# Kernel tuning notes

Measured on AMD Instinct MI355X. Metric: run time of the kernel, lower is better.

The kernel has to match this reference:

```python
import jax, jax.numpy as jnp
import numpy as np

DIM = 768
HEADS = 12
HEAD_DIM = DIM // HEADS
SCALE = HEAD_DIM ** -0.5


def setup_inputs() -> dict:
    key = jax.random.key(0)
    k1, k2, k3, k4 = jax.random.split(key, 4)
    x = jax.random.normal(k1, (1, 4096, DIM), dtype=jnp.float32)
    # qkv: Linear(dim, 3*dim), bias=False
    W_qkv = jax.random.normal(k2, (DIM, 3 * DIM), dtype=jnp.float32) * (DIM ** -0.5)
    # proj: Linear(dim, dim) with bias
    W_proj = jax.random.normal(k3, (DIM, DIM), dtype=jnp.float32) * (DIM ** -0.5)
    b_proj = jax.random.normal(k4, (DIM,), dtype=jnp.float32) * 0.01
    return {"x": x, "W_qkv": W_qkv, "W_proj": W_proj, "b_proj": b_proj}


def reference(x, W_qkv, W_proj, b_proj):
    b, n, d = x.shape
    qkv = x @ W_qkv                                  # [b, n, 3d]
    q, k, v = jnp.split(qkv, 3, axis=-1)             # each [b, n, d]
    # split heads: [b, n, (h hd)] -> [b, h, n, hd]
    def heads(t):
        return t.reshape(b, n, HEADS, HEAD_DIM).transpose(0, 2, 1, 3)
    q, k, v = heads(q) * SCALE, heads(k), heads(v)
    sim = jnp.einsum('bhid,bhjd->bhij', q, k)        # [b, h, n, n] -- full score matrix
    attn = jax.nn.softmax(sim, axis=-1)
    out = jnp.einsum('bhij,bhjd->bhid', attn, v)     # [b, h, n, hd]
    out = out.transpose(0, 2, 1, 3).reshape(b, n, d)  # merge heads
    return out @ W_proj + b_proj
```

## Files before the change

### kernel.cpp

```cpp
#include <hip/hip_runtime.h>
#include <math.h>

#define TOKENS 4096
#define DMODEL 768
#define NHEADS 12
#define HDIM   64
#define QKV_N  2304
#define ATTN_SCALE 0.125f
#define QSCALE_LOG2E (0.125f * 1.44269504088896340736f)

typedef __attribute__((ext_vector_type(8))) short bf16x8;
typedef __attribute__((ext_vector_type(4))) float floatx4;

__device__ __forceinline__ ushort f2bf(float f) {
    union { float f; unsigned u; } cv; cv.f = f;
    unsigned u = cv.u;
    u += 0x7fffu + ((u >> 16) & 1u);
    return (ushort)(u >> 16);
}

__device__ __forceinline__ unsigned cvt_pk_bf16(float a, float b) {
    unsigned r;
    asm("v_cvt_pk_bf16_f32 %0, %1, %2" : "=v"(r) : "v"(a), "v"(b));
    return r;
}

__device__ __forceinline__ void gl2lds16(const ushort* g, ushort* l) {
    __builtin_amdgcn_global_load_lds(
        (const __attribute__((address_space(1))) void*)g,
        (__attribute__((address_space(3))) void*)l, 16, 0, 0);
}

__device__ __forceinline__ bf16x8 frag(const ushort* ls, int row, int chunk) {
    return *(const bf16x8*)(ls + row * 64 + ((chunk ^ (row & 7)) * 8));
}

__global__ __launch_bounds__(256) void cvt_bf16_kernel(
    const float* __restrict__ in, ushort* __restrict__ out, int n4)
{
    const int i = blockIdx.x * 256 + threadIdx.x;
    if (i < n4) {
        const float4 v = ((const float4*)in)[i];
        ushort4 h;
        h.x = f2bf(v.x); h.y = f2bf(v.y); h.z = f2bf(v.z); h.w = f2bf(v.w);
        ((ushort4*)out)[i] = h;
    }
}

__global__ __launch_bounds__(256) void transpose_cvt_kernel(
    const float* __restrict__ in, ushort* __restrict__ out, int R, int C)
{
    __shared__ ushort tile[32][33];
    const int tx  = threadIdx.x & 31;
    const int ty8 = threadIdx.x >> 5;
    const int c0 = blockIdx.x * 32;
    const int r0 = blockIdx.y * 32;
    #pragma unroll
    for (int p = 0; p < 4; ++p) {
        const int r = ty8 + p * 8;
        tile[r][tx] = f2bf(in[(size_t)(r0 + r) * C + c0 + tx]);
    }
    __syncthreads();
    #pragma unroll
    for (int p = 0; p < 4; ++p) {
        const int c = ty8 + p * 8;
        out[(size_t)(c0 + c) * R + r0 + tx] = tile[tx][c];
    }
}

template<int NT>
__device__ __forceinline__ void gemm_body_async(
    const ushort* __restrict__ A, const ushort* __restrict__ Bt, int K,
    int m0, int n0, floatx4 acc[4][NT], ushort* ls)
{
    ushort* lsA = ls;
    ushort* lsB = ls + 8192;

    const int tid  = threadIdx.x;
    const int lane = tid & 63;
    const int wave = tid >> 6;
    const int wm = wave >> 1, wn = wave & 1;
    const int quad = lane >> 4, l16 = lane & 15;

    const int lrow = lane >> 3;
    const int csw  = ((lane & 7) ^ lrow) * 8;

    const ushort* gA = A  + (size_t)(m0 + wave * 32 + lrow) * K + csw;
    const ushort* gB = Bt + (size_t)(n0 + wave * NT * 8 + lrow) * K + csw;
    ushort* lA = lsA + (wave * 32) * 64;
    ushort* lB = lsB + (wave * NT * 8) * 64;

    for (int k0 = 0; k0 < K; k0 += 64) {
        __syncthreads();
        #pragma unroll
        for (int p = 0; p < 4; ++p)
            gl2lds16(gA + (size_t)p * 8 * K + k0, lA + p * 8 * 64);
        #pragma unroll
        for (int p = 0; p < NT; ++p)
            gl2lds16(gB + (size_t)p * 8 * K + k0, lB + p * 8 * 64);
        __syncthreads();

        #pragma unroll
        for (int ks = 0; ks < 2; ++ks) {
            bf16x8 af[4], bfr[NT];
            #pragma unroll
            for (int mt = 0; mt < 4; ++mt)
                af[mt] = frag(lsA, wm * 64 + mt * 16 + l16, ks * 4 + quad);
            #pragma unroll
            for (int nt = 0; nt < NT; ++nt)
                bfr[nt] = frag(lsB, wn * NT * 16 + nt * 16 + l16, ks * 4 + quad);
            #pragma unroll
            for (int mt = 0; mt < 4; ++mt)
                #pragma unroll
                for (int nt = 0; nt < NT; ++nt)
                    acc[mt][nt] = __builtin_amdgcn_mfma_f32_16x16x32_bf16(
                        af[mt], bfr[nt], acc[mt][nt], 0, 0, 0);
        }
    }
}

__global__ __launch_bounds__(256) void gemm_qkv_mfma(
    const ushort* __restrict__ Xb, const ushort* __restrict__ Wt,
    ushort* __restrict__ Qb, ushort* __restrict__ Kb, ushort* __restrict__ Vt)
{
    __shared__ __align__(16) ushort ls[16384];
    const int m0 = blockIdx.y * 128;
    const int n0 = blockIdx.x * 128;

    floatx4 acc[4][4] = {};
    gemm_body_async<4>(Xb, Wt, DMODEL, m0, n0, acc, ls);

    const int tid  = threadIdx.x;
    const int lane = tid & 63;
    const int wave = tid >> 6;
    const int wm = wave >> 1, wn = wave & 1;
    const int quad = lane >> 4, l16 = lane & 15;

    if (n0 < 2 * DMODEL) {
        const float scale = (n0 < DMODEL) ? QSCALE_LOG2E : 1.0f;
        ushort* outp = (n0 < DMODEL) ? Qb : Kb;
        const int colg = (n0 < DMODEL) ? n0 : n0 - DMODEL;
        #pragma unroll
        for (int p = 0; p < 2; ++p) {
            __syncthreads();
            if (wm == p) {
                #pragma unroll
                for (int mt = 0; mt < 4; ++mt)
                    #pragma unroll
                    for (int nt = 0; nt < 4; ++nt) {
                        const int row = mt * 16 + quad * 4;
                        const int col = wn * 64 + nt * 16 + l16;
                        #pragma unroll
                        for (int r = 0; r < 4; ++r)
                            ls[(row + r) * 136 + col] = f2bf(acc[mt][nt][r] * scale);
                    }
            }
            __syncthreads();
            #pragma unroll
            for (int p2 = 0; p2 < 4; ++p2) {
                const int row = (tid >> 4) + p2 * 16;
                const int c8  = (tid & 15) * 8;
                *(uint4*)(outp + (size_t)(m0 + p * 64 + row) * DMODEL + colg + c8) =
                    *(const uint4*)(ls + row * 136 + c8);
            }
        }
    } else {
        const int hd0 = n0 - 2 * DMODEL;
        #pragma unroll
        for (int p = 0; p < 2; ++p) {
            __syncthreads();
            if (wn == p) {
                #pragma unroll
                for (int mt = 0; mt < 4; ++mt)
                    #pragma unroll
                    for (int nt = 0; nt < 4; ++nt) {
                        const int hd  = nt * 16 + l16;
                        const int tok = wm * 64 + mt * 16 + quad * 4;
                        #pragma unroll
                        for (int r = 0; r < 4; ++r)
                            ls[hd * 136 + tok + r] = f2bf(acc[mt][nt][r]);
                    }
            }
            __syncthreads();
            #pragma unroll
            for (int p2 = 0; p2 < 4; ++p2) {
                const int row = (tid >> 4) + p2 * 16;
                const int c8  = (tid & 15) * 8;
                *(uint4*)(Vt + (size_t)(hd0 + p * 64 + row) * TOKENS + m0 + c8) =
                    *(const uint4*)(ls + row * 136 + c8);
            }
        }
    }
}

__global__ __launch_bounds__(256) void gemm_proj_mfma(
    const ushort* __restrict__ Ab, const ushort* __restrict__ Wt,
    const float* __restrict__ bias, float* __restrict__ out)
{
    __shared__ __align__(16) ushort ls[12288];
    const int m0 = blockIdx.y * 128;
    const int n0 = blockIdx.x * 64;

    floatx4 acc[4][2] = {};
    gemm_body_async<2>(Ab, Wt, DMODEL, m0, n0, acc, ls);

    const int lane = threadIdx.x & 63;
    const int wave = threadIdx.x >> 6;
    const int wm = wave >> 1, wn = wave & 1;
    const int quad = lane >> 4, l16 = lane & 15;
    const int row0 = m0 + wm * 64 + quad * 4;
    const int col0 = n0 + wn * 32;

    #pragma unroll
    for (int nt = 0; nt < 2; ++nt) {
        const int col = col0 + nt * 16 + l16;
        const float bv = bias[col];
        #pragma unroll
        for (int mt = 0; mt < 4; ++mt)
            #pragma unroll
            for (int r = 0; r < 4; ++r)
                out[(size_t)(row0 + mt * 16 + r) * DMODEL + col] =
                    acc[mt][nt][r] + bv;
    }
}

__global__ __launch_bounds__(256) void attn_mfma_kernel(
    const ushort* __restrict__ Qb, const ushort* __restrict__ Kb,
    const ushort* __restrict__ Vt, ushort* __restrict__ attn_out)
{
    __shared__ __align__(16) ushort lds[16384];

    const int tid  = threadIdx.x;
    const int wave = tid >> 6;
    const int lane = tid & 63;
    const int quad = lane >> 4;
    const int l16  = lane & 15;
    const int h    = blockIdx.y;
    const int i0   = blockIdx.x * 64;

    const ushort* qbase = Qb + (size_t)(i0 + wave * 16 + l16) * DMODEL + h * HDIM;
    const bf16x8 qf0 = *(const bf16x8*)(qbase + quad * 8);
    const bf16x8 qf1 = *(const bf16x8*)(qbase + 32 + quad * 8);

    bf16x8 ones;
    #pragma unroll
    for (int i = 0; i < 8; ++i) ones[i] = (short)0x3F80;

    floatx4 O[4] = {{0.f,0.f,0.f,0.f},{0.f,0.f,0.f,0.f},{0.f,0.f,0.f,0.f},{0.f,0.f,0.f,0.f}};
    floatx4 Ol = {0.f, 0.f, 0.f, 0.f};

    const int lrow = lane >> 3;
    const int csw  = ((lane & 7) ^ lrow) * 8;
    const ushort* gK = Kb + (size_t)(wave * 16 + lrow) * DMODEL + h * HDIM + csw;
    const ushort* gV = Vt + (size_t)(h * HDIM + wave * 16 + lrow) * TOKENS + csw;

    const int vhalf = (quad & 1) * 4;
    const int cb    = quad >> 1;

    #pragma unroll
    for (int p = 0; p < 2; ++p) {
        gl2lds16(gK + (size_t)p * 8 * DMODEL, lds + (wave * 16 + p * 8) * 64);
        gl2lds16(gV + (size_t)p * 8 * TOKENS, lds + 8192 + (wave * 16 + p * 8) * 64);
    }

    for (int j0 = 0; j0 < TOKENS; j0 += 64) {
        const int cur = (j0 >> 6) & 1;
        ushort* Ks = lds + cur * 4096;
        ushort* Vs = lds + 8192 + cur * 4096;
        ushort* Kn = lds + (1 - cur) * 4096;
        ushort* Vn = lds + 8192 + (1 - cur) * 4096;

        __syncthreads();

        if (j0 + 64 < TOKENS) {
            #pragma unroll
            for (int p = 0; p < 2; ++p) {
                gl2lds16(gK + (size_t)(j0 + 64) * DMODEL + (size_t)p * 8 * DMODEL,
                         Kn + (wave * 16 + p * 8) * 64);
                gl2lds16(gV + (size_t)(j0 + 64) + (size_t)p * 8 * TOKENS,
                         Vn + (wave * 16 + p * 8) * 64);
            }
        }

        floatx4 Sv[4];
        #pragma unroll
        for (int jt = 0; jt < 4; ++jt) {
            const bf16x8 k0 = frag(Ks, jt * 16 + l16, quad);
            const bf16x8 k1 = frag(Ks, jt * 16 + l16, 4 + quad);
            floatx4 s = {0.f, 0.f, 0.f, 0.f};
            s = __builtin_amdgcn_mfma_f32_16x16x32_bf16(k0, qf0, s, 0, 0, 0);
            s = __builtin_amdgcn_mfma_f32_16x16x32_bf16(k1, qf1, s, 0, 0, 0);
            Sv[jt] = s;
        }

        union { bf16x8 v; unsigned u[4]; } pf0u, pf1u;
        #pragma unroll
        for (int jt = 0; jt < 4; ++jt) {
            const float p0 = __builtin_amdgcn_exp2f(Sv[jt][0]);
            const float p1 = __builtin_amdgcn_exp2f(Sv[jt][1]);
            const float p2 = __builtin_amdgcn_exp2f(Sv[jt][2]);
            const float p3 = __builtin_amdgcn_exp2f(Sv[jt][3]);
            const unsigned w0 = cvt_pk_bf16(p0, p1);
            const unsigned w1 = cvt_pk_bf16(p2, p3);
            if (jt < 2) { pf0u.u[jt * 2] = w0;       pf0u.u[jt * 2 + 1] = w1; }
            else        { pf1u.u[(jt - 2) * 2] = w0; pf1u.u[(jt - 2) * 2 + 1] = w1; }
        }
        const bf16x8 pf0 = pf0u.v;
        const bf16x8 pf1 = pf1u.v;

        Ol = __builtin_amdgcn_mfma_f32_16x16x32_bf16(pf0, ones, Ol, 0, 0, 0);
        Ol = __builtin_amdgcn_mfma_f32_16x16x32_bf16(pf1, ones, Ol, 0, 0, 0);

        #pragma unroll
        for (int nt = 0; nt < 4; ++nt) {
            const int r = nt * 16 + l16;
            const ushort* vrow = Vs + r * 64 + vhalf;
            const int x = (r & 7);
            union { bf16x8 v; uint2 u[2]; } v0u, v1u;
            v0u.u[0] = *(const uint2*)(vrow + ((cb       ^ x) * 8));
            v0u.u[1] = *(const uint2*)(vrow + (((cb + 2) ^ x) * 8));
            v1u.u[0] = *(const uint2*)(vrow + (((cb + 4) ^ x) * 8));
            v1u.u[1] = *(const uint2*)(vrow + (((cb + 6) ^ x) * 8));
            O[nt] = __builtin_amdgcn_mfma_f32_16x16x32_bf16(pf0, v0u.v, O[nt], 0, 0, 0);
            O[nt] = __builtin_amdgcn_mfma_f32_16x16x32_bf16(pf1, v1u.v, O[nt], 0, 0, 0);
        }
    }

    float linv[4];
    #pragma unroll
    for (int r = 0; r < 4; ++r) linv[r] = __builtin_amdgcn_rcpf(Ol[r]);

    const int orow0 = i0 + wave * 16 + quad * 4;
    #pragma unroll
    for (int nt = 0; nt < 4; ++nt) {
        const int d = h * HDIM + nt * 16 + l16;
        #pragma unroll
        for (int r = 0; r < 4; ++r)
            attn_out[(size_t)(orow0 + r) * DMODEL + d] = f2bf(O[nt][r] * linv[r]);
    }
}

extern "C" void kernel_launch(void* const* d_in, const int* in_sizes, int n_in,
                              void* d_out, int out_size, void* d_ws, size_t ws_size,
                              hipStream_t stream)
{
    const float* x     = (const float*)d_in[0];
    const float* Wqkv  = (const float*)d_in[1];
    const float* Wproj = (const float*)d_in[2];
    const float* bproj = (const float*)d_in[3];
    float* out = (float*)d_out;

    ushort* Xb     = (ushort*)d_ws;
    ushort* WqkvT  = Xb    + (size_t)TOKENS * DMODEL;
    ushort* WprojT = WqkvT + (size_t)QKV_N * DMODEL;
    ushort* Qb     = WprojT + (size_t)DMODEL * DMODEL;
    ushort* Kb     = Qb    + (size_t)TOKENS * DMODEL;
    ushort* Vt     = Kb    + (size_t)TOKENS * DMODEL;
    ushort* attn   = Vt    + (size_t)TOKENS * DMODEL;

    cvt_bf16_kernel<<<dim3(TOKENS * DMODEL / 4 / 256), 256, 0, stream>>>(
        x, Xb, TOKENS * DMODEL / 4);
    transpose_cvt_kernel<<<dim3(QKV_N / 32, DMODEL / 32), 256, 0, stream>>>(
        Wqkv, WqkvT, DMODEL, QKV_N);
    transpose_cvt_kernel<<<dim3(DMODEL / 32, DMODEL / 32), 256, 0, stream>>>(
        Wproj, WprojT, DMODEL, DMODEL);

    gemm_qkv_mfma<<<dim3(QKV_N / 128, TOKENS / 128), 256, 0, stream>>>(
        Xb, WqkvT, Qb, Kb, Vt);

    attn_mfma_kernel<<<dim3(TOKENS / 64, NHEADS), 256, 0, stream>>>(
        Qb, Kb, Vt, attn);

    gemm_proj_mfma<<<dim3(DMODEL / 64, TOKENS / 128), 256, 0, stream>>>(
        attn, WprojT, bproj, out);
}
```

Before: 211.6 us.

## Split attention KV range across waves and reduce partial outputs in LDS

```diff
diff --git a/kernel.cpp b/kernel.cpp
--- a/kernel.cpp
+++ b/kernel.cpp
@@ -224,11 +224,11 @@
     }
 }
 
-__global__ __launch_bounds__(256) void attn_mfma_kernel(
+__global__ __launch_bounds__(256, 2) void attn_mfma_kernel(
     const ushort* __restrict__ Qb, const ushort* __restrict__ Kb,
     const ushort* __restrict__ Vt, ushort* __restrict__ attn_out)
 {
-    __shared__ __align__(16) ushort lds[16384];
+    __shared__ __align__(16) ushort lds[32768];
 
     const int tid  = threadIdx.x;
     const int wave = tid >> 6;
@@ -238,105 +238,160 @@
     const int h    = blockIdx.y;
     const int i0   = blockIdx.x * 64;
 
-    const ushort* qbase = Qb + (size_t)(i0 + wave * 16 + l16) * DMODEL + h * HDIM;
-    const bf16x8 qf0 = *(const bf16x8*)(qbase + quad * 8);
-    const bf16x8 qf1 = *(const bf16x8*)(qbase + 32 + quad * 8);
+    bf16x8 qf[4][2];
+    #pragma unroll
+    for (int jt = 0; jt < 4; ++jt) {
+        const ushort* qb = Qb + (size_t)(i0 + jt * 16 + l16) * DMODEL + h * HDIM;
+        qf[jt][0] = *(const bf16x8*)(qb + quad * 8);
+        qf[jt][1] = *(const bf16x8*)(qb + 32 + quad * 8);
+    }
 
     bf16x8 ones;
     #pragma unroll
     for (int i = 0; i < 8; ++i) ones[i] = (short)0x3F80;
 
-    floatx4 O[4] = {{0.f,0.f,0.f,0.f},{0.f,0.f,0.f,0.f},{0.f,0.f,0.f,0.f},{0.f,0.f,0.f,0.f}};
-    floatx4 Ol = {0.f, 0.f, 0.f, 0.f};
-
-    const int lrow = lane >> 3;
-    const int csw  = ((lane & 7) ^ lrow) * 8;
-    const ushort* gK = Kb + (size_t)(wave * 16 + lrow) * DMODEL + h * HDIM + csw;
-    const ushort* gV = Vt + (size_t)(h * HDIM + wave * 16 + lrow) * TOKENS + csw;
-
-    const int vhalf = (quad & 1) * 4;
-    const int cb    = quad >> 1;
-
-    #pragma unroll
-    for (int p = 0; p < 2; ++p) {
-        gl2lds16(gK + (size_t)p * 8 * DMODEL, lds + (wave * 16 + p * 8) * 64);
-        gl2lds16(gV + (size_t)p * 8 * TOKENS, lds + 8192 + (wave * 16 + p * 8) * 64);
-    }
-
-    for (int j0 = 0; j0 < TOKENS; j0 += 64) {
-        const int cur = (j0 >> 6) & 1;
-        ushort* Ks = lds + cur * 4096;
-        ushort* Vs = lds + 8192 + cur * 4096;
-        ushort* Kn = lds + (1 - cur) * 4096;
-        ushort* Vn = lds + 8192 + (1 - cur) * 4096;
+    floatx4 O[4][4] = {};
+    floatx4 Ol[4]   = {};
+
+    const int lrow8 = lane >> 3;
+    const int csw8  = ((lane & 7) ^ lrow8) * 8;
+    const ushort* gK = Kb + (size_t)(wave * 32 + lrow8) * DMODEL + h * HDIM + csw8;
+    const int l4 = lane >> 4;
+    const ushort* gVrow = Vt + (size_t)(h * HDIM + wave * 16 + l4) * TOKENS;
+
+    #pragma unroll
+    for (int p = 0; p < 4; ++p)
+        gl2lds16(gK + (size_t)p * 8 * DMODEL, lds + (wave * 32 + p * 8) * 64);
+    #pragma unroll
+    for (int p = 0; p < 4; ++p) {
+        const int vsw = ((lane & 15) ^ (p * 4 + l4)) * 8;
+        gl2lds16(gVrow + (size_t)(p * 4) * TOKENS + vsw,
+                 lds + 16384 + (wave * 16 + p * 4) * 128);
+    }
+
+    for (int j0 = 0; j0 < TOKENS; j0 += 128) {
+        const int cur = (j0 >> 7) & 1;
+        const ushort* Ks = lds + cur * 8192;
+        const ushort* Vs = lds + 16384 + cur * 8192;
+        ushort* Kn = lds + (1 - cur) * 8192;
+        ushort* Vn = lds + 16384 + (1 - cur) * 8192;
 
         __syncthreads();
 
-        if (j0 + 64 < TOKENS) {
-            #pragma unroll
-            for (int p = 0; p < 2; ++p) {
-                gl2lds16(gK + (size_t)(j0 + 64) * DMODEL + (size_t)p * 8 * DMODEL,
-                         Kn + (wave * 16 + p * 8) * 64);
-                gl2lds16(gV + (size_t)(j0 + 64) + (size_t)p * 8 * TOKENS,
-                         Vn + (wave * 16 + p * 8) * 64);
-            }
-        }
-
-        floatx4 Sv[4];
+        if (j0 + 128 < TOKENS) {
+            #pragma unroll
+            for (int p = 0; p < 4; ++p)
+                gl2lds16(gK + (size_t)(j0 + 128) * DMODEL + (size_t)p * 8 * DMODEL,
+                         Kn + (wave * 32 + p * 8) * 64);
+            #pragma unroll
+            for (int p = 0; p < 4; ++p) {
+                const int vsw = ((lane & 15) ^ (p * 4 + l4)) * 8;
+                gl2lds16(gVrow + (size_t)(p * 4) * TOKENS + (j0 + 128) + vsw,
+                         Vn + (wave * 16 + p * 4) * 128);
+            }
+        }
+
+        bf16x8 af[2][2];
+        #pragma unroll
+        for (int ks2 = 0; ks2 < 2; ++ks2)
+            #pragma unroll
+            for (int kh = 0; kh < 2; ++kh)
+                af[ks2][kh] = frag(Ks, wave * 32 + ks2 * 16 + l16, kh * 4 + quad);
+
+        bf16x8 vf[4];
+        #pragma unroll
+        for (int nt = 0; nt < 4; ++nt) {
+            const int vrow = nt * 16 + l16;
+            union { bf16x8 v; uint2 d[2]; } vu;
+            #pragma unroll
+            for (int ks2 = 0; ks2 < 2; ++ks2) {
+                const int t   = wave * 4 + ks2 * 2 + (quad >> 1);
+                const int pos = t ^ (vrow & 15);
+                vu.d[ks2] = *(const uint2*)(Vs + vrow * 128 + pos * 8 + (quad & 1) * 4);
+            }
+            vf[nt] = vu.v;
+        }
+
+        floatx4 Sv[4][2];
+        #pragma unroll
+        for (int jt = 0; jt < 4; ++jt)
+            #pragma unroll
+            for (int ks2 = 0; ks2 < 2; ++ks2) {
+                floatx4 s = {0.f, 0.f, 0.f, 0.f};
+                s = __builtin_amdgcn_mfma_f32_16x16x32_bf16(af[ks2][0], qf[jt][0], s, 0, 0, 0);
+                s = __builtin_amdgcn_mfma_f32_16x16x32_bf16(af[ks2][1], qf[jt][1], s, 0, 0, 0);
+                Sv[jt][ks2] = s;
+            }
+
+        bf16x8 pa[4];
         #pragma unroll
         for (int jt = 0; jt < 4; ++jt) {
-            const bf16x8 k0 = frag(Ks, jt * 16 + l16, quad);
-            const bf16x8 k1 = frag(Ks, jt * 16 + l16, 4 + quad);
-            floatx4 s = {0.f, 0.f, 0.f, 0.f};
-            s = __builtin_amdgcn_mfma_f32_16x16x32_bf16(k0, qf0, s, 0, 0, 0);
-            s = __builtin_amdgcn_mfma_f32_16x16x32_bf16(k1, qf1, s, 0, 0, 0);
-            Sv[jt] = s;
-        }
-
-        union { bf16x8 v; unsigned u[4]; } pf0u, pf1u;
+            union { bf16x8 v; unsigned u[4]; } pu;
+            #pragma unroll
+            for (int ks2 = 0; ks2 < 2; ++ks2) {
+                const float p0 = __builtin_amdgcn_exp2f(Sv[jt][ks2][0]);
+                const float p1 = __builtin_amdgcn_exp2f(Sv[jt][ks2][1]);
+                const float p2 = __builtin_amdgcn_exp2f(Sv[jt][ks2][2]);
+                const float p3 = __builtin_amdgcn_exp2f(Sv[jt][ks2][3]);
+                pu.u[ks2 * 2]     = cvt_pk_bf16(p0, p1);
+                pu.u[ks2 * 2 + 1] = cvt_pk_bf16(p2, p3);
+            }
+            pa[jt] = pu.v;
+            Ol[jt] = __builtin_amdgcn_mfma_f32_16x16x32_bf16(pa[jt], ones, Ol[jt], 0, 0, 0);
+        }
+
+        #pragma unroll
+        for (int jt = 0; jt < 4; ++jt)
+            #pragma unroll
+            for (int nt = 0; nt < 4; ++nt)
+                O[jt][nt] = __builtin_amdgcn_mfma_f32_16x16x32_bf16(
+                    pa[jt], vf[nt], O[jt][nt], 0, 0, 0);
+    }
+
+    __syncthreads();
+    float* Of  = (float*)lds;
+    float* Olf = ((float*)lds) + 3 * 64 * 66;
+    if (wave != 0) {
+        const int rg = (wave - 1) * 64 * 66;
         #pragma unroll
         for (int jt = 0; jt < 4; ++jt) {
-            const float p0 = __builtin_amdgcn_exp2f(Sv[jt][0]);
-            const float p1 = __builtin_amdgcn_exp2f(Sv[jt][1]);
-            const float p2 = __builtin_amdgcn_exp2f(Sv[jt][2]);
-            const float p3 = __builtin_amdgcn_exp2f(Sv[jt][3]);
-            const unsigned w0 = cvt_pk_bf16(p0, p1);
-            const unsigned w1 = cvt_pk_bf16(p2, p3);
-            if (jt < 2) { pf0u.u[jt * 2] = w0;       pf0u.u[jt * 2 + 1] = w1; }
-            else        { pf1u.u[(jt - 2) * 2] = w0; pf1u.u[(jt - 2) * 2 + 1] = w1; }
-        }
-        const bf16x8 pf0 = pf0u.v;
-        const bf16x8 pf1 = pf1u.v;
-
-        Ol = __builtin_amdgcn_mfma_f32_16x16x32_bf16(pf0, ones, Ol, 0, 0, 0);
-        Ol = __builtin_amdgcn_mfma_f32_16x16x32_bf16(pf1, ones, Ol, 0, 0, 0);
-
-        #pragma unroll
-        for (int nt = 0; nt < 4; ++nt) {
-            const int r = nt * 16 + l16;
-            const ushort* vrow = Vs + r * 64 + vhalf;
-            const int x = (r & 7);
-            union { bf16x8 v; uint2 u[2]; } v0u, v1u;
-            v0u.u[0] = *(const uint2*)(vrow + ((cb       ^ x) * 8));
-            v0u.u[1] = *(const uint2*)(vrow + (((cb + 2) ^ x) * 8));
-            v1u.u[0] = *(const uint2*)(vrow + (((cb + 4) ^ x) * 8));
-            v1u.u[1] = *(const uint2*)(vrow + (((cb + 6) ^ x) * 8));
-            O[nt] = __builtin_amdgcn_mfma_f32_16x16x32_bf16(pf0, v0u.v, O[nt], 0, 0, 0);
-            O[nt] = __builtin_amdgcn_mfma_f32_16x16x32_bf16(pf1, v1u.v, O[nt], 0, 0, 0);
-        }
-    }
-
-    float linv[4];
-    #pragma unroll
-    for (int r = 0; r < 4; ++r) linv[r] = __builtin_amdgcn_rcpf(Ol[r]);
-
-    const int orow0 = i0 + wave * 16 + quad * 4;
-    #pragma unroll
-    for (int nt = 0; nt < 4; ++nt) {
-        const int d = h * HDIM + nt * 16 + l16;
-        #pragma unroll
-        for (int r = 0; r < 4; ++r)
-            attn_out[(size_t)(orow0 + r) * DMODEL + d] = f2bf(O[nt][r] * linv[r]);
+            #pragma unroll
+            for (int nt = 0; nt < 4; ++nt)
+                #pragma unroll
+                for (int r = 0; r < 4; ++r)
+                    Of[rg + (jt * 16 + quad * 4 + r) * 66 + nt * 16 + l16] = O[jt][nt][r];
+            if (l16 == 0) {
+                #pragma unroll
+                for (int r = 0; r < 4; ++r)
+                    Olf[(wave - 1) * 64 + jt * 16 + quad * 4 + r] = Ol[jt][r];
+            }
+        }
+    }
+    __syncthreads();
+    if (wave == 0) {
+        #pragma unroll
+        for (int jt = 0; jt < 4; ++jt) {
+            const int qr = jt * 16 + quad * 4;
+            float linv[4];
+            #pragma unroll
+            for (int r = 0; r < 4; ++r) {
+                const float l = Ol[jt][r] + Olf[qr + r] + Olf[64 + qr + r]
+                              + Olf[128 + qr + r];
+                linv[r] = __builtin_amdgcn_rcpf(l);
+            }
+            #pragma unroll
+            for (int nt = 0; nt < 4; ++nt) {
+                const int d = h * HDIM + nt * 16 + l16;
+                #pragma unroll
+                for (int r = 0; r < 4; ++r) {
+                    const float o = O[jt][nt][r]
+                        + Of[(qr + r) * 66 + nt * 16 + l16]
+                        + Of[64 * 66 + (qr + r) * 66 + nt * 16 + l16]
+                        + Of[2 * 64 * 66 + (qr + r) * 66 + nt * 16 + l16];
+                    attn_out[(size_t)(i0 + qr + r) * DMODEL + d] = f2bf(o * linv[r]);
+                }
+            }
+        }
     }
 }
 
```

After: 216.1 us. +2.1%, slower.
